# Kernel optimization log

Measured on AMD Instinct MI355X. Metric: run time of the kernel, lower is better.

The kernel has to match this reference:

```python
import jax, jax.numpy as jnp
import numpy as np

D_K = 24
ALPHA = 0.1
N_HEADS = 6
D_MODEL = 144
LN_EPS = 1e-5


def setup_inputs() -> dict:
    key = jax.random.key(0)
    ks = jax.random.split(key, 8)
    B, S = 8, 2048
    Q = jax.random.normal(ks[0], (B, S, D_MODEL), dtype=jnp.float32)
    K = jax.random.normal(ks[1], (B, N_HEADS, S, D_K), dtype=jnp.float32)
    V = jax.random.normal(ks[2], (B, N_HEADS, S, D_K), dtype=jnp.float32)
    attn_mask = jax.random.randint(ks[3], (B, S, S), 0, 2).astype(bool)
    Wq_w = jax.random.normal(ks[4], (D_MODEL, D_MODEL), dtype=jnp.float32) * 0.05
    Wq_b = jnp.zeros((D_MODEL,), dtype=jnp.float32)
    lin_w = jax.random.normal(ks[5], (D_MODEL, D_MODEL), dtype=jnp.float32) * 0.05
    lin_b = jnp.zeros((D_MODEL,), dtype=jnp.float32)
    ln_g = jnp.ones((D_MODEL,), dtype=jnp.float32)
    ln_b = jnp.zeros((D_MODEL,), dtype=jnp.float32)
    return {"Q": Q, "K": K, "V": V, "attn_mask": attn_mask,
            "Wq_w": Wq_w, "Wq_b": Wq_b, "lin_w": lin_w, "lin_b": lin_b,
            "ln_g": ln_g, "ln_b": ln_b}


def reference(Q, K, V, attn_mask, Wq_w, Wq_b, lin_w, lin_b, ln_g, ln_b):
    B, S, _ = Q.shape
    residual = Q
    # W_Q projection then head split: [B,S,D] -> [B,H,S,d_k]
    q = (Q @ Wq_w.T + Wq_b).reshape(B, S, N_HEADS, D_K).transpose(0, 2, 1, 3)
    # scores [B,H,S,Sk]; custom tanh activation instead of softmax
    scores = jnp.einsum('bhqd,bhkd->bhqk', q, K) / np.sqrt(D_K).astype(np.float32)
    attn = jnp.tanh(ALPHA * scores)
    # NOTE: original calls attn.masked_fill(...) non-inplace and drops the
    # result, so attn_mask has no effect. Faithfully ignored here.
    context = jnp.einsum('bhqk,bhkd->bhqd', attn, V)
    context = context.transpose(0, 2, 1, 3).reshape(B, S, N_HEADS * D_K)
    output = context @ lin_w.T + lin_b
    x = output + residual
    mu = jnp.mean(x, axis=-1, keepdims=True)
    var = jnp.var(x, axis=-1, keepdims=True)
    return (x - mu) / jnp.sqrt(var + LN_EPS) * ln_g + ln_b
```

## Files before the change

### kernel.cpp

```cpp
#include <hip/hip_runtime.h>
#include <hip/hip_bf16.h>

#define B_  8
#define S_  2048
#define H_  6
#define DK_ 24
#define DM_ 144

#define TK0  2.0412414523193153e-02f
#define TK1 -2.8350575726379381e-06f
#define TK2  4.7250959543965635e-10f

typedef __bf16 bf16x8 __attribute__((ext_vector_type(8)));
typedef __bf16 bf16x2 __attribute__((ext_vector_type(2)));
typedef float  f32x4  __attribute__((ext_vector_type(4)));
typedef float  f32x2  __attribute__((ext_vector_type(2)));

#define MFMA_ __builtin_amdgcn_mfma_f32_16x16x32_bf16

__device__ __forceinline__ unsigned short f2bf(float f) {
    return __builtin_bit_cast(unsigned short, (__bf16)f);
}
__device__ __forceinline__ uint pack2(float a, float b) {
    bf16x2 v; v[0] = (__bf16)a; v[1] = (__bf16)b;
    return __builtin_bit_cast(uint, v);
}
__device__ __forceinline__ uint tanh2_pack(float a, float b) {
    f32x2 c; c[0] = a; c[1] = b;
    f32x2 t = c * c;
    f32x2 u = t * TK2 + TK1;
    u = t * u + TK0;
    f32x2 r = c * u;
    return pack2(r[0], r[1]);
}

__device__ __forceinline__ void swap32(uint &x, uint &y) {
    auto r = __builtin_amdgcn_permlane32_swap(x, y, false, false);
    x = r[0]; y = r[1];
}
__device__ __forceinline__ void swap16(uint &x, uint &y, bool hi16) {
#if __has_builtin(__builtin_amdgcn_permlane16_swap)
    (void)hi16;
    auto r = __builtin_amdgcn_permlane16_swap(x, y, false, false);
    x = r[0]; y = r[1];
#else
    uint xs = __builtin_amdgcn_ds_swizzle(x, 0x401F);
    uint ys = __builtin_amdgcn_ds_swizzle(y, 0x401F);
    uint nx = hi16 ? ys : x;
    uint ny = hi16 ? y : xs;
    x = nx; y = ny;
#endif
}

__global__ __launch_bounds__(256)
void prep_kernel(const float* __restrict__ K, const float* __restrict__ V,
                 const float* __restrict__ Wq, const float* __restrict__ Wqb,
                 const float* __restrict__ Wl, const float* __restrict__ lb,
                 ushort* __restrict__ Ktt, ushort* __restrict__ Vtt,
                 ushort* __restrict__ Whq, ushort* __restrict__ Wlp) {
    __shared__ float sv[64 * 25];
    const int t = threadIdx.x;
    const int bid = blockIdx.x;
    if (bid >= 1536) {
        int i = (bid - 1536) * 256 + t;
        if (i < 30720) {
            int h = i / 5120, rem = i % 5120;
            int d = rem / 160, c = rem % 160;
            float v = 0.f;
            if (d < DK_) {
                if (c < DM_)       v = Wq[(h * DK_ + d) * DM_ + c];
                else if (c == DM_) v = Wqb[h * DK_ + d];
            }
            Whq[i] = f2bf(v);
        } else if (i < 53760) {
            int j = i - 30720;
            int r = j / 160, c = j % 160;
            float v = (c < DM_) ? Wl[r * DM_ + c] : (c == DM_ ? lb[r] : 0.f);
            Wlp[j] = f2bf(v);
        }
        return;
    }
    const int kt = bid & 31, h = (bid >> 5) % H_, b = bid / (32 * H_);
    const int bh = b * H_ + h;
    const size_t tile = (size_t)(bh * 32 + kt);
    const float4* Ks = (const float4*)(K + ((size_t)bh * S_ + kt * 64) * DK_);
    ushort* Ko = Ktt + tile * 2048;
    for (int idx = t; idx < 384; idx += 256) {
        int r = idx / 6, c4 = (idx % 6) * 4;
        float4 v = Ks[idx];
        ushort4 u; u.x = f2bf(v.x); u.y = f2bf(v.y); u.z = f2bf(v.z); u.w = f2bf(v.w);
        *(ushort4*)&Ko[r * 32 + c4] = u;
    }
    if (t < 64) { uint4 z = {0u,0u,0u,0u}; *(uint4*)&Ko[t * 32 + 24] = z; }
    const float4* Vs = (const float4*)(V + ((size_t)bh * S_ + kt * 64) * DK_);
    for (int idx = t; idx < 384; idx += 256) {
        int r = idx / 6, c4 = (idx % 6) * 4;
        *(float4*)&sv[r * 25 + c4] = Vs[idx];
    }
    __syncthreads();
    int d = t >> 3, s8 = (t & 7) * 8;
    uint4 o = {0u,0u,0u,0u};
    if (d < DK_) {
        o.x = pack2(sv[(s8 + 0) * 25 + d], sv[(s8 + 1) * 25 + d]);
        o.y = pack2(sv[(s8 + 2) * 25 + d], sv[(s8 + 3) * 25 + d]);
        o.z = pack2(sv[(s8 + 4) * 25 + d], sv[(s8 + 5) * 25 + d]);
        o.w = pack2(sv[(s8 + 6) * 25 + d], sv[(s8 + 7) * 25 + d]);
    }
    ((uint4*)Vtt)[tile * 256 + t] = o;
}

__global__ __launch_bounds__(512, 6)
void attn_kernel(const float* __restrict__ Q, const ushort* __restrict__ Whq,
                 const ushort* __restrict__ Ktt, const ushort* __restrict__ Vtt,
                 ushort* __restrict__ Cb) {
    __shared__ __attribute__((aligned(16))) char smem[19456];
    ushort* s_q  = (ushort*)smem;
    ushort* s_vt = (ushort*)(smem + 10240);
    float*  s_ctx = (float*)smem;

    const int t = threadIdx.x;
    const int w = t >> 6, n16 = t & 15, g = (t >> 4) & 3;
    const bool hi16 = (t & 16) != 0;
    const int qp = blockIdx.x, h = blockIdx.y, b = blockIdx.z;
    const int bh = b * H_ + h;
    const int row0 = qp * 128;

    const uint4* Kb4 = (const uint4*)Ktt + (size_t)bh * 8192;
    const uint2* Vb2 = (const uint2*)Vtt + (size_t)bh * 16384;

    const int stoff = (t >> 4) * 72 + (t & 15) * 4;
    uint2 vreg = Vb2[t];

    const f32x4 zf = {0.f, 0.f, 0.f, 0.f};
    const uint4* Wh4 = (const uint4*)Whq + h * 640;
    {
        const float* Qr = Q + (size_t)(b * S_ + row0 + w * 16 + n16) * DM_;
        f32x4 qa0 = zf, qa1 = zf;
#pragma unroll
        for (int ks = 0; ks < 5; ++ks) {
            bf16x8 av;
            if (ks < 4 || g < 2) {
                float4 f0 = *(const float4*)&Qr[ks * 32 + g * 8];
                float4 f1 = *(const float4*)&Qr[ks * 32 + g * 8 + 4];
                uint4 u;
                u.x = pack2(f0.x, f0.y); u.y = pack2(f0.z, f0.w);
                u.z = pack2(f1.x, f1.y); u.w = pack2(f1.z, f1.w);
                av = __builtin_bit_cast(bf16x8, u);
            } else {
                uint4 u = {0u, 0u, 0u, 0u};
                if (g == 2) u.x = 0x00003F80u;
                av = __builtin_bit_cast(bf16x8, u);
            }
            bf16x8 bv0 = __builtin_bit_cast(bf16x8, Wh4[n16 * 20 + ks * 4 + g]);
            bf16x8 bv1 = __builtin_bit_cast(bf16x8, Wh4[(16 + n16) * 20 + ks * 4 + g]);
            qa0 = MFMA_(av, bv0, qa0, 0, 0, 0);
            qa1 = MFMA_(av, bv1, qa1, 0, 0, 0);
        }
#pragma unroll
        for (int reg = 0; reg < 4; ++reg) {
            int r = (w * 16 + g * 4 + reg) * 40;
            s_q[r + n16]      = f2bf(qa0[reg]);
            s_q[r + 16 + n16] = f2bf(qa1[reg]);
        }
    }
    const bf16x8 qf = *(const bf16x8*)&s_q[(w * 16 + n16) * 40 + g * 8];

    const int koff = n16 * 4 + g;
    const int voff = n16 * 72 + g * 8;
    f32x4 acc0 = zf, acc1 = zf;

    auto phase = [&](ushort* vbuf, int ktile) {
        *(uint2*)&vbuf[stoff] = vreg;
        __syncthreads();
        vreg = Vb2[(((ktile + 1) & 31) << 9) + t];
        const uint4* Kt4 = Kb4 + (ktile << 8);
        bf16x8 a0 = __builtin_bit_cast(bf16x8, Kt4[koff]);
        bf16x8 a1 = __builtin_bit_cast(bf16x8, Kt4[koff + 64]);
        bf16x8 a2 = __builtin_bit_cast(bf16x8, Kt4[koff + 128]);
        bf16x8 a3 = __builtin_bit_cast(bf16x8, Kt4[koff + 192]);
        __builtin_amdgcn_s_setprio(1);
        f32x4 c0 = MFMA_(a0, qf, zf, 0, 0, 0);
        f32x4 c1 = MFMA_(a1, qf, zf, 0, 0, 0);
        f32x4 c2 = MFMA_(a2, qf, zf, 0, 0, 0);
        f32x4 c3 = MFMA_(a3, qf, zf, 0, 0, 0);
        __builtin_amdgcn_s_setprio(0);
        uint W0p0 = tanh2_pack(c0[0], c0[1]);
        uint W0p1 = tanh2_pack(c0[2], c0[3]);
        uint W1p0 = tanh2_pack(c1[0], c1[1]);
        uint W1p1 = tanh2_pack(c1[2], c1[3]);
        uint W2p0 = tanh2_pack(c2[0], c2[1]);
        uint W2p1 = tanh2_pack(c2[2], c2[3]);
        uint W3p0 = tanh2_pack(c3[0], c3[1]);
        uint W3p1 = tanh2_pack(c3[2], c3[3]);
        swap32(W0p0, W1p0);
        swap32(W2p0, W3p0);
        swap32(W0p1, W1p1);
        swap32(W2p1, W3p1);
        swap16(W0p0, W1p0, hi16);
        swap16(W2p0, W3p0, hi16);
        swap16(W0p1, W1p1, hi16);
        swap16(W2p1, W3p1, hi16);
        uint4 ap0u, ap1u;
        ap0u.x = W0p0; ap0u.y = W0p1; ap0u.z = W1p0; ap0u.w = W1p1;
        ap1u.x = W2p0; ap1u.y = W2p1; ap1u.z = W3p0; ap1u.w = W3p1;
        bf16x8 ap0 = __builtin_bit_cast(bf16x8, ap0u);
        bf16x8 ap1 = __builtin_bit_cast(bf16x8, ap1u);
        bf16x8 vb00 = *(const bf16x8*)&vbuf[voff];
        bf16x8 vb01 = *(const bf16x8*)&vbuf[voff + 32];
        bf16x8 vb10 = *(const bf16x8*)&vbuf[1152 + voff];
        bf16x8 vb11 = *(const bf16x8*)&vbuf[1152 + voff + 32];
        __builtin_amdgcn_s_setprio(1);
        acc0 = MFMA_(ap0, vb00, acc0, 0, 0, 0);
        acc0 = MFMA_(ap1, vb01, acc0, 0, 0, 0);
        acc1 = MFMA_(ap0, vb10, acc1, 0, 0, 0);
        acc1 = MFMA_(ap1, vb11, acc1, 0, 0, 0);
        __builtin_amdgcn_s_setprio(0);
    };
    for (int kt = 0; kt < 32; kt += 2) {
        phase(s_vt, kt);
        phase(s_vt + 2304, kt + 1);
    }

    __syncthreads();
#pragma unroll
    for (int reg = 0; reg < 4; ++reg) {
        int row = w * 16 + g * 4 + reg;
        s_ctx[row * 28 + n16] = acc0[reg];
        if (n16 < 8) s_ctx[row * 28 + 16 + n16] = acc1[reg];
    }
    __syncthreads();
    if (t < 384) {
        int r = t / 3, c = t % 3;
        const float* src = &s_ctx[r * 28 + c * 8];
        uint4 u;
        u.x = pack2(src[0], src[1]); u.y = pack2(src[2], src[3]);
        u.z = pack2(src[4], src[5]); u.w = pack2(src[6], src[7]);
        *(uint4*)&Cb[(size_t)(b * S_ + row0 + r) * 160 + h * 24 + c * 8] = u;
    }
}

__global__ __launch_bounds__(512)
void outln_kernel(const float* __restrict__ Qres, const ushort* __restrict__ Wlp,
                  const ushort* __restrict__ Cb,
                  const float* __restrict__ lg, const float* __restrict__ lbeta,
                  float* __restrict__ io) {
    __shared__ __attribute__((aligned(16))) ushort s_a[64 * 168];
    __shared__ __attribute__((aligned(16))) ushort s_w[144 * 168];
    __shared__ float s_red[2][2][64];
    const int t = threadIdx.x;
    const int w = t >> 6, n16 = t & 15, g = (t >> 4) & 3;
    const int wq = w & 3, half = w >> 2;
    const int nt_base = half * 5, nt_cnt = half ? 4 : 5;
    const int row0 = blockIdx.x * 64;

    const ushort* Cr = Cb + (size_t)row0 * 160;
    for (int idx = t; idx < 1152; idx += 512) {
        int r = idx / 18, c8 = (idx % 18) * 8;
        *(uint4*)&s_a[r * 168 + c8] = *(const uint4*)&Cr[r * 160 + c8];
    }
    if (t < 64) {
        uint4 pad = {0x00003F80u, 0u, 0u, 0u};
        uint4 z4  = {0u, 0u, 0u, 0u};
        *(uint4*)&s_a[t * 168 + 144] = pad;
        *(uint4*)&s_a[t * 168 + 152] = z4;
    }
    for (int idx = t; idx < 2880; idx += 512) {
        int r = idx / 20, c8 = (idx % 20) * 8;
        *(uint4*)&s_w[r * 168 + c8] = *(const uint4*)&Wlp[r * 160 + c8];
    }
    __syncthreads();

    f32x4 acc[5];
#pragma unroll
    for (int j = 0; j < 5; ++j) acc[j] = (f32x4){0.f, 0.f, 0.f, 0.f};
#pragma unroll
    for (int ks = 0; ks < 5; ++ks) {
        bf16x8 av = *(const bf16x8*)&s_a[(wq * 16 + n16) * 168 + ks * 32 + g * 8];
        for (int j = 0; j < nt_cnt; ++j) {
            bf16x8 bv = *(const bf16x8*)&s_w[((nt_base + j) * 16 + n16) * 168 + ks * 32 + g * 8];
            acc[j] = MFMA_(av, bv, acc[j], 0, 0, 0);
        }
    }
    float vals[5][4], s1[4] = {0, 0, 0, 0}, s2[4] = {0, 0, 0, 0};
    for (int j = 0; j < nt_cnt; ++j) {
        int d = (nt_base + j) * 16 + n16;
#pragma unroll
        for (int reg = 0; reg < 4; ++reg) {
            int row = row0 + wq * 16 + g * 4 + reg;
            float v = acc[j][reg] + Qres[(size_t)row * DM_ + d];
            vals[j][reg] = v;
            s1[reg] += v; s2[reg] = fmaf(v, v, s2[reg]);
        }
    }
#pragma unroll
    for (int off = 1; off < 16; off <<= 1) {
#pragma unroll
        for (int reg = 0; reg < 4; ++reg) {
            s1[reg] += __shfl_xor(s1[reg], off);
            s2[reg] += __shfl_xor(s2[reg], off);
        }
    }
    if (n16 == 0) {
#pragma unroll
        for (int reg = 0; reg < 4; ++reg) {
            int rr = wq * 16 + g * 4 + reg;
            s_red[half][0][rr] = s1[reg];
            s_red[half][1][rr] = s2[reg];
        }
    }
    __syncthreads();
    float mu[4], rs[4];
#pragma unroll
    for (int reg = 0; reg < 4; ++reg) {
        int rr = wq * 16 + g * 4 + reg;
        float S1 = s_red[0][0][rr] + s_red[1][0][rr];
        float S2 = s_red[0][1][rr] + s_red[1][1][rr];
        float m = S1 * (1.f / 144.f);
        mu[reg] = m;
        rs[reg] = rsqrtf(S2 * (1.f / 144.f) - m * m + 1e-5f);
    }
    for (int j = 0; j < nt_cnt; ++j) {
        int d = (nt_base + j) * 16 + n16;
        float gv = lg[d], bv = lbeta[d];
#pragma unroll
        for (int reg = 0; reg < 4; ++reg) {
            int row = row0 + wq * 16 + g * 4 + reg;
            io[(size_t)row * DM_ + d] = (vals[j][reg] - mu[reg]) * rs[reg] * gv + bv;
        }
    }
}

extern "C" void kernel_launch(void* const* d_in, const int* in_sizes, int n_in,
                              void* d_out, int out_size, void* d_ws, size_t ws_size,
                              hipStream_t stream) {
    const float* Q     = (const float*)d_in[0];
    const float* K     = (const float*)d_in[1];
    const float* V     = (const float*)d_in[2];
    const float* Wq_w  = (const float*)d_in[4];
    const float* Wq_b  = (const float*)d_in[5];
    const float* lin_w = (const float*)d_in[6];
    const float* lin_b = (const float*)d_in[7];
    const float* ln_g  = (const float*)d_in[8];
    const float* ln_b  = (const float*)d_in[9];
    float* out = (float*)d_out;

    ushort* Ktt = (ushort*)d_ws;
    ushort* Vtt = (ushort*)((char*)d_ws + 6291456);
    ushort* Whq = (ushort*)((char*)d_ws + 12582912);
    ushort* Wlp = (ushort*)((char*)d_ws + 12644352);
    ushort* Cb  = (ushort*)((char*)d_ws + 12690432);

    prep_kernel<<<1746, 256, 0, stream>>>(K, V, Wq_w, Wq_b, lin_w, lin_b,
                                          Ktt, Vtt, Whq, Wlp);
    attn_kernel<<<dim3(S_ / 128, H_, B_), 512, 0, stream>>>(Q, Whq, Ktt, Vtt, Cb);
    outln_kernel<<<(B_ * S_) / 64, 512, 0, stream>>>(Q, Wlp, Cb, ln_g, ln_b, out);
}
```

Before: 271.3 us.

## Double query rows per attention block and stage K tiles through LDS

```diff
diff --git a/kernel.cpp b/kernel.cpp
--- a/kernel.cpp
+++ b/kernel.cpp
@@ -109,13 +109,14 @@
     ((uint4*)Vtt)[tile * 256 + t] = o;
 }
 
-__global__ __launch_bounds__(512, 6)
+__global__ __launch_bounds__(512, 4)
 void attn_kernel(const float* __restrict__ Q, const ushort* __restrict__ Whq,
                  const ushort* __restrict__ Ktt, const ushort* __restrict__ Vtt,
                  ushort* __restrict__ Cb) {
-    __shared__ __attribute__((aligned(16))) char smem[19456];
+    __shared__ __attribute__((aligned(16))) char smem[39936];
     ushort* s_q  = (ushort*)smem;
-    ushort* s_vt = (ushort*)(smem + 10240);
+    ushort* s_k  = (ushort*)(smem + 20480);
+    ushort* s_vt = (ushort*)(smem + 30720);
     float*  s_ctx = (float*)smem;
 
     const int t = threadIdx.x;
@@ -123,18 +124,21 @@
     const bool hi16 = (t & 16) != 0;
     const int qp = blockIdx.x, h = blockIdx.y, b = blockIdx.z;
     const int bh = b * H_ + h;
-    const int row0 = qp * 128;
+    const int row0 = qp * 256;
 
     const uint4* Kb4 = (const uint4*)Ktt + (size_t)bh * 8192;
-    const uint2* Vb2 = (const uint2*)Vtt + (size_t)bh * 16384;
-
-    const int stoff = (t >> 4) * 72 + (t & 15) * 4;
-    uint2 vreg = Vb2[t];
+    const uint4* Vb4 = (const uint4*)Vtt + (size_t)bh * 8192;
+
+    const int t2 = t & 255;
+    const int stoff = (t < 256) ? ((t2 >> 2) * 40 + (t2 & 3) * 8)
+                                : ((t2 >> 3) * 72 + (t2 & 7) * 8);
+    uint4 sreg = (t < 256) ? Kb4[t2] : Vb4[t2];
 
     const f32x4 zf = {0.f, 0.f, 0.f, 0.f};
     const uint4* Wh4 = (const uint4*)Whq + h * 640;
-    {
-        const float* Qr = Q + (size_t)(b * S_ + row0 + w * 16 + n16) * DM_;
+#pragma unroll
+    for (int hf = 0; hf < 2; ++hf) {
+        const float* Qr = Q + (size_t)(b * S_ + row0 + w * 32 + hf * 16 + n16) * DM_;
         f32x4 qa0 = zf, qa1 = zf;
 #pragma unroll
         for (int ks = 0; ks < 5; ++ks) {
@@ -158,31 +162,34 @@
         }
 #pragma unroll
         for (int reg = 0; reg < 4; ++reg) {
-            int r = (w * 16 + g * 4 + reg) * 40;
+            int r = (w * 32 + hf * 16 + g * 4 + reg) * 40;
             s_q[r + n16]      = f2bf(qa0[reg]);
             s_q[r + 16 + n16] = f2bf(qa1[reg]);
         }
     }
-    const bf16x8 qf = *(const bf16x8*)&s_q[(w * 16 + n16) * 40 + g * 8];
-
-    const int koff = n16 * 4 + g;
+    const bf16x8 qf0 = *(const bf16x8*)&s_q[(w * 32 + n16) * 40 + g * 8];
+    const bf16x8 qf1 = *(const bf16x8*)&s_q[(w * 32 + 16 + n16) * 40 + g * 8];
+
+    const int aoff = n16 * 40 + g * 8;
     const int voff = n16 * 72 + g * 8;
-    f32x4 acc0 = zf, acc1 = zf;
-
-    auto phase = [&](ushort* vbuf, int ktile) {
-        *(uint2*)&vbuf[stoff] = vreg;
+    f32x4 acc00 = zf, acc01 = zf, acc10 = zf, acc11 = zf;
+
+    auto phase = [&](ushort* kbuf, ushort* vbuf, int ktile) {
+        *(uint4*)(((t < 256) ? kbuf : vbuf) + stoff) = sreg;
         __syncthreads();
-        vreg = Vb2[(((ktile + 1) & 31) << 9) + t];
-        const uint4* Kt4 = Kb4 + (ktile << 8);
-        bf16x8 a0 = __builtin_bit_cast(bf16x8, Kt4[koff]);
-        bf16x8 a1 = __builtin_bit_cast(bf16x8, Kt4[koff + 64]);
-        bf16x8 a2 = __builtin_bit_cast(bf16x8, Kt4[koff + 128]);
-        bf16x8 a3 = __builtin_bit_cast(bf16x8, Kt4[koff + 192]);
+        {
+            int nt = ((ktile + 1) & 31) * 256;
+            sreg = (t < 256) ? Kb4[nt + t2] : Vb4[nt + t2];
+        }
+        bf16x8 a0 = *(const bf16x8*)&kbuf[aoff];
+        bf16x8 a1 = *(const bf16x8*)&kbuf[640 + aoff];
+        bf16x8 a2 = *(const bf16x8*)&kbuf[1280 + aoff];
+        bf16x8 a3 = *(const bf16x8*)&kbuf[1920 + aoff];
         __builtin_amdgcn_s_setprio(1);
-        f32x4 c0 = MFMA_(a0, qf, zf, 0, 0, 0);
-        f32x4 c1 = MFMA_(a1, qf, zf, 0, 0, 0);
-        f32x4 c2 = MFMA_(a2, qf, zf, 0, 0, 0);
-        f32x4 c3 = MFMA_(a3, qf, zf, 0, 0, 0);
+        f32x4 c0 = MFMA_(a0, qf0, zf, 0, 0, 0);
+        f32x4 c1 = MFMA_(a1, qf0, zf, 0, 0, 0);
+        f32x4 c2 = MFMA_(a2, qf0, zf, 0, 0, 0);
+        f32x4 c3 = MFMA_(a3, qf0, zf, 0, 0, 0);
         __builtin_amdgcn_s_setprio(0);
         uint W0p0 = tanh2_pack(c0[0], c0[1]);
         uint W0p1 = tanh2_pack(c0[2], c0[3]);
@@ -200,37 +207,70 @@
         swap16(W2p0, W3p0, hi16);
         swap16(W0p1, W1p1, hi16);
         swap16(W2p1, W3p1, hi16);
-        uint4 ap0u, ap1u;
-        ap0u.x = W0p0; ap0u.y = W0p1; ap0u.z = W1p0; ap0u.w = W1p1;
-        ap1u.x = W2p0; ap1u.y = W2p1; ap1u.z = W3p0; ap1u.w = W3p1;
-        bf16x8 ap0 = __builtin_bit_cast(bf16x8, ap0u);
-        bf16x8 ap1 = __builtin_bit_cast(bf16x8, ap1u);
+        uint4 apu;
+        apu.x = W0p0; apu.y = W0p1; apu.z = W1p0; apu.w = W1p1;
+        bf16x8 ap0h0 = __builtin_bit_cast(bf16x8, apu);
+        apu.x = W2p0; apu.y = W2p1; apu.z = W3p0; apu.w = W3p1;
+        bf16x8 ap1h0 = __builtin_bit_cast(bf16x8, apu);
+        __builtin_amdgcn_s_setprio(1);
+        c0 = MFMA_(a0, qf1, zf, 0, 0, 0);
+        c1 = MFMA_(a1, qf1, zf, 0, 0, 0);
+        c2 = MFMA_(a2, qf1, zf, 0, 0, 0);
+        c3 = MFMA_(a3, qf1, zf, 0, 0, 0);
+        __builtin_amdgcn_s_setprio(0);
+        W0p0 = tanh2_pack(c0[0], c0[1]);
+        W0p1 = tanh2_pack(c0[2], c0[3]);
+        W1p0 = tanh2_pack(c1[0], c1[1]);
+        W1p1 = tanh2_pack(c1[2], c1[3]);
+        W2p0 = tanh2_pack(c2[0], c2[1]);
+        W2p1 = tanh2_pack(c2[2], c2[3]);
+        W3p0 = tanh2_pack(c3[0], c3[1]);
+        W3p1 = tanh2_pack(c3[2], c3[3]);
+        swap32(W0p0, W1p0);
+        swap32(W2p0, W3p0);
+        swap32(W0p1, W1p1);
+        swap32(W2p1, W3p1);
+        swap16(W0p0, W1p0, hi16);
+        swap16(W2p0, W3p0, hi16);
+        swap16(W0p1, W1p1, hi16);
+        swap16(W2p1, W3p1, hi16);
+        apu.x = W0p0; apu.y = W0p1; apu.z = W1p0; apu.w = W1p1;
+        bf16x8 ap0h1 = __builtin_bit_cast(bf16x8, apu);
+        apu.x = W2p0; apu.y = W2p1; apu.z = W3p0; apu.w = W3p1;
+        bf16x8 ap1h1 = __builtin_bit_cast(bf16x8, apu);
         bf16x8 vb00 = *(const bf16x8*)&vbuf[voff];
         bf16x8 vb01 = *(const bf16x8*)&vbuf[voff + 32];
         bf16x8 vb10 = *(const bf16x8*)&vbuf[1152 + voff];
         bf16x8 vb11 = *(const bf16x8*)&vbuf[1152 + voff + 32];
         __builtin_amdgcn_s_setprio(1);
-        acc0 = MFMA_(ap0, vb00, acc0, 0, 0, 0);
-        acc0 = MFMA_(ap1, vb01, acc0, 0, 0, 0);
-        acc1 = MFMA_(ap0, vb10, acc1, 0, 0, 0);
-        acc1 = MFMA_(ap1, vb11, acc1, 0, 0, 0);
+        acc00 = MFMA_(ap0h0, vb00, acc00, 0, 0, 0);
+        acc00 = MFMA_(ap1h0, vb01, acc00, 0, 0, 0);
+        acc01 = MFMA_(ap0h0, vb10, acc01, 0, 0, 0);
+        acc01 = MFMA_(ap1h0, vb11, acc01, 0, 0, 0);
+        acc10 = MFMA_(ap0h1, vb00, acc10, 0, 0, 0);
+        acc10 = MFMA_(ap1h1, vb01, acc10, 0, 0, 0);
+        acc11 = MFMA_(ap0h1, vb10, acc11, 0, 0, 0);
+        acc11 = MFMA_(ap1h1, vb11, acc11, 0, 0, 0);
         __builtin_amdgcn_s_setprio(0);
     };
     for (int kt = 0; kt < 32; kt += 2) {
-        phase(s_vt, kt);
-        phase(s_vt + 2304, kt + 1);
+        phase(s_k, s_vt, kt);
+        phase(s_k + 2560, s_vt + 2304, kt + 1);
     }
 
     __syncthreads();
 #pragma unroll
     for (int reg = 0; reg < 4; ++reg) {
-        int row = w * 16 + g * 4 + reg;
-        s_ctx[row * 28 + n16] = acc0[reg];
-        if (n16 < 8) s_ctx[row * 28 + 16 + n16] = acc1[reg];
-    }
-    __syncthreads();
-    if (t < 384) {
-        int r = t / 3, c = t % 3;
+        int r0 = w * 32 + g * 4 + reg;
+        s_ctx[r0 * 28 + n16] = acc00[reg];
+        if (n16 < 8) s_ctx[r0 * 28 + 16 + n16] = acc01[reg];
+        int r1 = r0 + 16;
+        s_ctx[r1 * 28 + n16] = acc10[reg];
+        if (n16 < 8) s_ctx[r1 * 28 + 16 + n16] = acc11[reg];
+    }
+    __syncthreads();
+    for (int idx = t; idx < 768; idx += 512) {
+        int r = idx / 3, c = idx % 3;
         const float* src = &s_ctx[r * 28 + c * 8];
         uint4 u;
         u.x = pack2(src[0], src[1]); u.y = pack2(src[2], src[3]);
@@ -352,6 +392,6 @@
 
     prep_kernel<<<1746, 256, 0, stream>>>(K, V, Wq_w, Wq_b, lin_w, lin_b,
                                           Ktt, Vtt, Whq, Wlp);
-    attn_kernel<<<dim3(S_ / 128, H_, B_), 512, 0, stream>>>(Q, Whq, Ktt, Vtt, Cb);
+    attn_kernel<<<dim3(S_ / 256, H_, B_), 512, 0, stream>>>(Q, Whq, Ktt, Vtt, Cb);
     outln_kernel<<<(B_ * S_) / 64, 512, 0, stream>>>(Q, Wlp, Cb, ln_g, ln_b, out);
 }
```

New measurement: 263.7 us. 2.8% less time.
